# Performance work log

Measured on AMD Instinct MI355X. Metric: run time of the kernel, lower is better.

The kernel has to match this reference:

```python
import jax, jax.numpy as jnp
import numpy as np

S, B, H = 2048, 2, 2048
NP = 16            # num attention heads
HN = H // NP       # head dim = 128


def setup_inputs() -> dict:
    key = jax.random.key(0)
    k0, k1, k2 = jax.random.split(key, 3)
    hidden_states = jax.random.normal(k0, (S, B, H), dtype=jnp.float32) * 0.02
    w_qkv = jax.random.normal(k1, (3 * H, H), dtype=jnp.float32) * 0.02
    b_qkv = jnp.zeros((3 * H,), dtype=jnp.float32)
    w_dense = jax.random.normal(k2, (H, H), dtype=jnp.float32) * 0.02
    b_dense = jnp.zeros((H,), dtype=jnp.float32)
    # causal mask: True means "mask out" (strictly upper triangular)
    attention_mask = jnp.triu(jnp.ones((S, S), dtype=bool), k=1)[None, None]  # [1,1,S,S]
    return {
        "hidden_states": hidden_states,
        "attention_mask": attention_mask,
        "w_qkv": w_qkv,
        "b_qkv": b_qkv,
        "w_dense": w_dense,
        "b_dense": b_dense,
    }


def reference(hidden_states, attention_mask, w_qkv, b_qkv, w_dense, b_dense):
    s, b, h = hidden_states.shape
    # fused QKV projection (ColumnParallelLinear: y = x @ W^T + b)
    mixed = hidden_states @ w_qkv.T + b_qkv                 # [s,b,3h]
    mixed = mixed.reshape(s, b, NP, 3 * HN)
    q, k, v = jnp.split(mixed, 3, axis=-1)                  # each [s,b,np,hn]
    norm = 1.0 / jnp.sqrt(jnp.asarray(HN, hidden_states.dtype))
    # scaled QK^T -> [b,np,sq,sk]
    scores = jnp.einsum("sbnh,tbnh->bnst", q, k) * norm
    # attention_mask_func: masked_fill(mask, -10000.0)
    scores = jnp.where(attention_mask, jnp.asarray(-10000.0, scores.dtype), scores)
    # softmax in fp32 (softmax_in_fp32)
    probs = jax.nn.softmax(scores.astype(jnp.float32), axis=-1).astype(scores.dtype)
    # AV matmul -> [s,b,np,hn] -> [s,b,h]
    context = jnp.einsum("bnst,tbnh->sbnh", probs, v).reshape(s, b, h)
    # output projection (RowParallelLinear)
    out = context @ w_dense.T + b_dense
    return out
```

## Files before the change

kernel.cpp:

```cpp
#include <hip/hip_runtime.h>
#include <hip/hip_bf16.h>
#include <cstdint>
#include <cstddef>

#define SS   2048
#define BB   2
#define HH   2048
#define NHEAD 16
#define HDIM 128
#define H3   6144
#define MROWS 4096

typedef __attribute__((ext_vector_type(4))) float f32x4;
typedef __attribute__((ext_vector_type(8))) __bf16 bf16x8;
typedef __attribute__((ext_vector_type(8))) unsigned short us8;
typedef __attribute__((ext_vector_type(4))) unsigned short us4;

__device__ __forceinline__ unsigned short f2b(float f) {
    union { float f; unsigned u; } v; v.f = f;
    unsigned r = v.u + 0x7fffu + ((v.u >> 16) & 1u);
    return (unsigned short)(r >> 16);
}

__device__ __forceinline__ unsigned short f2b_hw(float f) {
    return __builtin_bit_cast(unsigned short, (__bf16)f);
}

__device__ __forceinline__ float exp2_fast(float x) {
    float r;
    asm("v_exp_f32 %0, %1" : "=v"(r) : "v"(x));
    return r;
}

__device__ __forceinline__ bf16x8 ld_b16x8(const unsigned short* p) {
    us8 u = *(const us8*)p;
    return __builtin_bit_cast(bf16x8, u);
}

__device__ __forceinline__ bf16x8 ld8_off(const unsigned short* base, int byteoff) {
    return __builtin_bit_cast(bf16x8, *(const us8*)((const char*)base + byteoff));
}

__device__ __forceinline__ int sw256(int b) { return b ^ (((b >> 8) & 7) << 4); }
__device__ __forceinline__ int sw128(int b) { return b ^ (((b >> 7) & 7) << 4); }

__device__ __forceinline__ void gload_lds16(const unsigned short* g, unsigned short* l) {
    __builtin_amdgcn_global_load_lds(
        (const __attribute__((address_space(1))) unsigned int*)g,
        (__attribute__((address_space(3))) unsigned int*)l, 16, 0, 0);
}

__global__ __launch_bounds__(256) void cvt_f32_bf16(
    const float* __restrict__ in, unsigned short* __restrict__ out, int n4)
{
    const int stride = gridDim.x * blockDim.x;
    for (int i = blockIdx.x * blockDim.x + threadIdx.x; i < n4; i += stride) {
        const float4 v = ((const float4*)in)[i];
        us4 o = { f2b(v.x), f2b(v.y), f2b(v.z), f2b(v.w) };
        ((us4*)out)[i] = o;
    }
}

__global__ __launch_bounds__(256) void transpose_v(
    const unsigned short* __restrict__ mixed,
    unsigned short* __restrict__ vt)
{
    const int st = blockIdx.x;
    const int nh = blockIdx.y;
    const int bb = blockIdx.z;
    const int tid = threadIdx.x;
    __shared__ unsigned short T[64][136];
#pragma unroll
    for (int i = 0; i < 4; ++i) {
        const int c = i * 256 + tid;
        const int sl = c >> 4, d0 = (c & 15) << 3;
        const us8 v = *(const us8*)(mixed +
            ((size_t)(st * 64 + sl) * BB + bb) * H3 + nh * 384 + 256 + d0);
        *(us8*)(&T[sl][d0]) = v;
    }
    __syncthreads();
#pragma unroll
    for (int i = 0; i < 4; ++i) {
        const int c = i * 256 + tid;
        const int d = c >> 3, sl0 = (c & 7) << 3;
        us8 o;
#pragma unroll
        for (int j = 0; j < 8; ++j) o[j] = T[sl0 + j][d];
        *(us8*)(vt + ((size_t)(bb * NHEAD + nh) * HDIM + d) * SS + st * 64 + sl0) = o;
    }
}

#define STAGE_UNIT(gp, lo)                                        \
    gload_lds16((gp) + soff[0], smem + (lo) + tid * 8);           \
    gload_lds16((gp) + soff[1], smem + (lo) + 4096 + tid * 8);

template <int BN, bool F32OUT>
__global__ __launch_bounds__(512, 2) void gemm_8ph(
    const unsigned short* __restrict__ A,
    const unsigned short* __restrict__ Bw,
    const float* __restrict__ bias,
    void* __restrict__ Cout,
    int Nv, int Kv)
{
    extern __shared__ unsigned short smem[];
    constexpr int NF     = BN / 64;
    constexpr int BUNITS = BN / 128;
    constexpr int BELEMS = BN * 64;

    const int tid  = threadIdx.x;
    const int lane = tid & 63;
    const int wave = tid >> 6;
    const int wm = wave >> 2, wn = wave & 3;
    const int bm = blockIdx.y, bn = blockIdx.x;

    const unsigned short* Ab = A  + (size_t)bm * 128 * Kv;
    const unsigned short* Bb = Bw + (size_t)bn * BN * Kv;

    int soff[2];
#pragma unroll
    for (int i = 0; i < 2; ++i) {
        const int p = (i * 512 + tid) * 16;
        const int l = p ^ (((p >> 7) & 7) << 4);
        soff[i] = (l >> 7) * Kv + ((l & 127) >> 1);
    }

    f32x4 acc[4][NF];
#pragma unroll
    for (int m = 0; m < 4; ++m)
#pragma unroll
        for (int n = 0; n < NF; ++n) acc[m][n] = (f32x4){0.f, 0.f, 0.f, 0.f};

    const int frow = lane & 15;
    const int g16  = (lane >> 4) << 4;
    const int swx  = (frow & 7) << 4;
    const int kx0  = g16 ^ swx;
    const int kx1  = (64 + g16) ^ swx;
    const int aRow = (wm * 64 + frow) * 128;
    const int bRow = 32768 + (wn * (BN / 4) + frow) * 128;

    const int NT = Kv >> 6;

    STAGE_UNIT(Ab, 0);
    STAGE_UNIT(Bb, 16384);
    STAGE_UNIT(Bb + 128 * Kv, 16384 + 8192);
    if constexpr (BUNITS == 3) { STAGE_UNIT(Bb + 256 * Kv, 16384 + 16384); }
    STAGE_UNIT(Bb + 64, 16384 + BELEMS);
    STAGE_UNIT(Bb + 128 * Kv + 64, 16384 + BELEMS + 8192);
    if constexpr (BUNITS == 3) { STAGE_UNIT(Bb + 256 * Kv + 64, 16384 + BELEMS + 16384); }
    if constexpr (BUNITS == 3) { asm volatile("s_waitcnt vmcnt(6)" ::: "memory"); }
    else                       { asm volatile("s_waitcnt vmcnt(4)" ::: "memory"); }
    __builtin_amdgcn_s_barrier();

    for (int t = 0; t < NT; ++t) {
        const int j  = t & 1;
        const int jn = j ^ 1;
        const int aj = j * 16384;
        const int bj = j * (BN * 128);
        const int cA = ((t + 1 < NT) ? (t + 1) : (NT - 1)) * 64;
        const int cB = ((t + 2 < NT) ? (t + 2) : (NT - 1)) * 64;

        bf16x8 bbf[NF][2];

        {
            bf16x8 a0 = ld8_off(smem, aj + aRow + 0 * 2048 + kx0);
            bf16x8 a1 = ld8_off(smem, aj + aRow + 0 * 2048 + kx1);
#pragma unroll
            for (int n = 0; n < NF; ++n) {
                bbf[n][0] = ld8_off(smem, bj + bRow + n * 2048 + kx0);
                bbf[n][1] = ld8_off(smem, bj + bRow + n * 2048 + kx1);
            }
            STAGE_UNIT(Ab + cA, jn * 8192);
            __builtin_amdgcn_s_barrier();
            asm volatile("s_waitcnt lgkmcnt(0)" ::: "memory");
            __builtin_amdgcn_sched_barrier(0);
            __builtin_amdgcn_s_setprio(1);
#pragma unroll
            for (int n = 0; n < NF; ++n) {
                acc[0][n] = __builtin_amdgcn_mfma_f32_16x16x32_bf16(a0, bbf[n][0], acc[0][n], 0, 0, 0);
                acc[0][n] = __builtin_amdgcn_mfma_f32_16x16x32_bf16(a1, bbf[n][1], acc[0][n], 0, 0, 0);
            }
            __builtin_amdgcn_s_setprio(0);
        }
        {
            bf16x8 a0 = ld8_off(smem, aj + aRow + 1 * 2048 + kx0);
            bf16x8 a1 = ld8_off(smem, aj + aRow + 1 * 2048 + kx1);
            STAGE_UNIT(Bb + cB, 16384 + j * BELEMS);
            __builtin_amdgcn_s_barrier();
            asm volatile("s_waitcnt lgkmcnt(0)" ::: "memory");
            __builtin_amdgcn_sched_barrier(0);
            __builtin_amdgcn_s_setprio(1);
#pragma unroll
            for (int n = 0; n < NF; ++n) {
                acc[1][n] = __builtin_amdgcn_mfma_f32_16x16x32_bf16(a0, bbf[n][0], acc[1][n], 0, 0, 0);
                acc[1][n] = __builtin_amdgcn_mfma_f32_16x16x32_bf16(a1, bbf[n][1], acc[1][n], 0, 0, 0);
            }
            __builtin_amdgcn_s_setprio(0);
        }
        {
            bf16x8 a0 = ld8_off(smem, aj + aRow + 2 * 2048 + kx0);
            bf16x8 a1 = ld8_off(smem, aj + aRow + 2 * 2048 + kx1);
            STAGE_UNIT(Bb + 128 * Kv + cB, 16384 + j * BELEMS + 8192);
            __builtin_amdgcn_s_barrier();
            asm volatile("s_waitcnt lgkmcnt(0)" ::: "memory");
            __builtin_amdgcn_sched_barrier(0);
            __builtin_amdgcn_s_setprio(1);
#pragma unroll
            for (int n = 0; n < NF; ++n) {
                acc[2][n] = __builtin_amdgcn_mfma_f32_16x16x32_bf16(a0, bbf[n][0], acc[2][n], 0, 0, 0);
                acc[2][n] = __builtin_amdgcn_mfma_f32_16x16x32_bf16(a1, bbf[n][1], acc[2][n], 0, 0, 0);
            }
            __builtin_amdgcn_s_setprio(0);
        }
        {
            bf16x8 a0 = ld8_off(smem, aj + aRow + 3 * 2048 + kx0);
            bf16x8 a1 = ld8_off(smem, aj + aRow + 3 * 2048 + kx1);
            if constexpr (BUNITS == 3) {
                STAGE_UNIT(Bb + 256 * Kv + cB, 16384 + j * BELEMS + 16384);
            }
            __builtin_amdgcn_s_barrier();
            asm volatile("s_waitcnt lgkmcnt(0)" ::: "memory");
            __builtin_amdgcn_sched_barrier(0);
            __builtin_amdgcn_s_setprio(1);
#pragma unroll
            for (int n = 0; n < NF; ++n) {
                acc[3][n] = __builtin_amdgcn_mfma_f32_16x16x32_bf16(a0, bbf[n][0], acc[3][n], 0, 0, 0);
                acc[3][n] = __builtin_amdgcn_mfma_f32_16x16x32_bf16(a1, bbf[n][1], acc[3][n], 0, 0, 0);
            }
            __builtin_amdgcn_s_setprio(0);
            if constexpr (BUNITS == 3) { asm volatile("s_waitcnt vmcnt(6)" ::: "memory"); }
            else                       { asm volatile("s_waitcnt vmcnt(4)" ::: "memory"); }
        }
    }

    const int r0 = (lane >> 4) << 2;
#pragma unroll
    for (int m = 0; m < 4; ++m) {
        const int row = bm * 128 + wm * 64 + m * 16 + r0;
#pragma unroll
        for (int n = 0; n < NF; ++n) {
            const int col = bn * BN + wn * (BN / 4) + n * 16 + frow;
            const float bv = bias[col];
            float scale = 1.0f;
            if constexpr (!F32OUT) {
                if ((col % 384) < 128)
                    scale = (float)(0.08838834764831843 * 1.4426950408889634);
            }
#pragma unroll
            for (int r = 0; r < 4; ++r) {
                const float o = (acc[m][n][r] + bv) * scale;
                if (F32OUT) ((float*)Cout)[(size_t)(row + r) * Nv + col] = o;
                else        ((unsigned short*)Cout)[(size_t)(row + r) * Nv + col] = f2b(o);
            }
        }
    }
}

__global__ __launch_bounds__(256) void attn_kernel(
    const unsigned short* __restrict__ mixed,
    const unsigned short* __restrict__ vt,
    unsigned short* __restrict__ context)
{
    const int id   = blockIdx.x;
    const int c    = id & 7;
    const int k    = id >> 3;
    const int pair = k & 15;
    const int nhbb = c + 8 * (k >> 4);
    const int nh   = nhbb >> 1;
    const int bb   = nhbb & 1;

    const int tid  = threadIdx.x;
    const int lane = tid & 63;
    const int wave = tid >> 6;

    __shared__ __align__(1024) unsigned short smem[16384 + 16384 + 4096];

    const int frow = lane & 15;
    const int g16  = (lane >> 4) << 4;
    const int r0   = (lane >> 4) << 2;

    int koff[4], voff[4];
#pragma unroll
    for (int i = 0; i < 4; ++i) {
        const int p0 = (i * 256 + tid) * 16;
        const int lK = p0 ^ (((p0 >> 8) & 7) << 4);
        koff[i] = (lK >> 8) * (BB * H3) + ((lK & 255) >> 1);
        const int lV = p0 ^ (((p0 >> 7) & 7) << 4);
        voff[i] = (lV >> 7) * SS + ((lV & 127) >> 1);
    }

    const unsigned short* kg = mixed + (size_t)bb * H3 + nh * 384 + 128;
    const unsigned short* vg = vt + (size_t)(bb * NHEAD + nh) * HDIM * SS;

    char* Pb = (char*)(smem + 32768) + wave * 2048;

    for (int half = 0; half < 2; ++half) {
        const int qt = half ? (31 - pair) : pair;
        const int q0 = qt * 64 + wave * 16;

        bf16x8 qf[4];
        {
            const unsigned short* qptr =
                mixed + ((size_t)(q0 + frow) * BB + bb) * H3 + nh * 384;
#pragma unroll
            for (int kk = 0; kk < 4; ++kk)
                qf[kk] = ld_b16x8(qptr + kk * 32 + ((lane >> 4) << 3));
        }

        f32x4 Oacc[8];
#pragma unroll
        for (int ct = 0; ct < 8; ++ct) Oacc[ct] = (f32x4){0.f, 0.f, 0.f, 0.f};
        float m_r[4] = {-1e30f, -1e30f, -1e30f, -1e30f};
        float l_r[4] = {0.f, 0.f, 0.f, 0.f};

        {
            unsigned short* Kd = smem + wave * 512;
            unsigned short* Vd = smem + 16384 + wave * 512;
#pragma unroll
            for (int i = 0; i < 4; ++i) {
                gload_lds16(kg + koff[i], Kd + i * 2048);
                gload_lds16(vg + voff[i], Vd + i * 2048);
            }
        }
        __syncthreads();

        int cur = 0;
        for (int kt = 0; kt <= qt; ++kt) {
            if (kt < qt) {
                const unsigned short* kt_g = kg + (size_t)(kt + 1) * 64 * (BB * H3);
                const unsigned short* vt_g = vg + (kt + 1) * 64;
                unsigned short* Kd = smem + (cur ^ 1) * 8192 + wave * 512;
                unsigned short* Vd = smem + 16384 + (cur ^ 1) * 8192 + wave * 512;
#pragma unroll
                for (int i = 0; i < 4; ++i) {
                    gload_lds16(kt_g + koff[i], Kd + i * 2048);
                    gload_lds16(vt_g + voff[i], Vd + i * 2048);
                }
            }

            const unsigned short* Ks = smem + cur * 8192;
            const unsigned short* Vs = smem + 16384 + cur * 8192;

            f32x4 sc4[4];
#pragma unroll
            for (int t = 0; t < 4; ++t) {
                f32x4 s = (f32x4){0.f, 0.f, 0.f, 0.f};
#pragma unroll
                for (int kk = 0; kk < 4; ++kk) {
                    bf16x8 kf = ld8_off(Ks, sw256((t * 16 + frow) * 256 + kk * 64 + g16));
                    s = __builtin_amdgcn_mfma_f32_16x16x32_bf16(qf[kk], kf, s, 0, 0, 0);
                }
                sc4[t] = s;
            }

            if (kt == qt) {
#pragma unroll
                for (int t = 0; t < 4; ++t) {
                    const int kcol = qt * 64 + t * 16 + frow;
#pragma unroll
                    for (int r = 0; r < 4; ++r)
                        if (kcol > q0 + r0 + r) sc4[t][r] = -1e30f;
                }
            }

            float pmax[4];
#pragma unroll
            for (int r = 0; r < 4; ++r)
                pmax[r] = fmaxf(fmaxf(sc4[0][r], sc4[1][r]), fmaxf(sc4[2][r], sc4[3][r]));
            bool need = false;
#pragma unroll
            for (int r = 0; r < 4; ++r) need = need || (pmax[r] > m_r[r] + 11.5f);
            if (__any(need)) {
                float tmax[4];
#pragma unroll
                for (int r = 0; r < 4; ++r) {
                    tmax[r] = pmax[r];
                    tmax[r] = fmaxf(tmax[r], __shfl_xor(tmax[r], 1, 64));
                    tmax[r] = fmaxf(tmax[r], __shfl_xor(tmax[r], 2, 64));
                    tmax[r] = fmaxf(tmax[r], __shfl_xor(tmax[r], 4, 64));
                    tmax[r] = fmaxf(tmax[r], __shfl_xor(tmax[r], 8, 64));
                }
                float a_r[4];
#pragma unroll
                for (int r = 0; r < 4; ++r) {
                    const float mnew = fmaxf(m_r[r], tmax[r]);
                    a_r[r] = exp2_fast(m_r[r] - mnew);
                    m_r[r] = mnew;
                    l_r[r] *= a_r[r];
                }
#pragma unroll
                for (int ct = 0; ct < 8; ++ct)
#pragma unroll
                    for (int r = 0; r < 4; ++r) Oacc[ct][r] *= a_r[r];
            }

            float rsum[4] = {0.f, 0.f, 0.f, 0.f};
#pragma unroll
            for (int t = 0; t < 4; ++t)
#pragma unroll
                for (int r = 0; r < 4; ++r) {
                    const float p = exp2_fast(sc4[t][r] - m_r[r]);
                    sc4[t][r] = p;
                    rsum[r] += p;
                }
#pragma unroll
            for (int r = 0; r < 4; ++r) {
                rsum[r] += __shfl_xor(rsum[r], 1, 64);
                rsum[r] += __shfl_xor(rsum[r], 2, 64);
                rsum[r] += __shfl_xor(rsum[r], 4, 64);
                rsum[r] += __shfl_xor(rsum[r], 8, 64);
                l_r[r] += rsum[r];
            }

#pragma unroll
            for (int t = 0; t < 4; ++t)
#pragma unroll
                for (int r = 0; r < 4; ++r)
                    *(unsigned short*)(Pb + sw128((r0 + r) * 128 + (t * 16 + frow) * 2)) =
                        f2b_hw(sc4[t][r]);

#pragma unroll
            for (int ks = 0; ks < 2; ++ks) {
                bf16x8 pf = ld8_off((const unsigned short*)Pb, sw128(frow * 128 + ks * 64 + g16));
#pragma unroll
                for (int ct = 0; ct < 8; ++ct) {
                    bf16x8 vf = ld8_off(Vs, sw128((ct * 16 + frow) * 128 + ks * 64 + g16));
                    Oacc[ct] = __builtin_amdgcn_mfma_f32_16x16x32_bf16(pf, vf, Oacc[ct], 0, 0, 0);
                }
            }

            __syncthreads();
            cur ^= 1;
        }

#pragma unroll
        for (int ct = 0; ct < 8; ++ct) {
            const int d = ct * 16 + frow;
#pragma unroll
            for (int r = 0; r < 4; ++r) {
                const float o = Oacc[ct][r] / l_r[r];
                const size_t row = (size_t)(q0 + r0 + r) * BB + bb;
                context[row * HH + nh * 128 + d] = f2b_hw(o);
            }
        }
    }
}

extern "C" void kernel_launch(void* const* d_in, const int* in_sizes, int n_in,
                              void* d_out, int out_size, void* d_ws, size_t ws_size,
                              hipStream_t stream) {
    const float* hidden  = (const float*)d_in[0];
    const float* w_qkv   = (const float*)d_in[2];
    const float* b_qkv   = (const float*)d_in[3];
    const float* w_dense = (const float*)d_in[4];
    const float* b_dense = (const float*)d_in[5];
    float* out = (float*)d_out;

    unsigned short* mixed = (unsigned short*)d_ws;
    unsigned short* hb    = mixed + (size_t)MROWS * H3;
    unsigned short* wq    = hb + (size_t)MROWS * HH;
    unsigned short* wd    = wq + (size_t)H3 * HH;
    unsigned short* context = hb;
    unsigned short* vtg     = wq;

    dim3 blk(256);
    cvt_f32_bf16<<<2048, blk, 0, stream>>>(hidden, hb, (MROWS * HH) / 4);
    cvt_f32_bf16<<<2048, blk, 0, stream>>>(w_qkv, wq, (H3 * HH) / 4);
    cvt_f32_bf16<<<1024, blk, 0, stream>>>(w_dense, wd, (HH * HH) / 4);

    hipFuncSetAttribute(reinterpret_cast<const void*>(gemm_8ph<384, false>),
                        hipFuncAttributeMaxDynamicSharedMemorySize, 131072);
    gemm_8ph<384, false><<<dim3(H3 / 384, MROWS / 128), dim3(512), 131072, stream>>>(
        hb, wq, b_qkv, mixed, H3, HH);
    transpose_v<<<dim3(32, NHEAD, BB), blk, 0, stream>>>(mixed, vtg);
    attn_kernel<<<dim3(512), blk, 0, stream>>>(mixed, vtg, context);
    hipFuncSetAttribute(reinterpret_cast<const void*>(gemm_8ph<256, true>),
                        hipFuncAttributeMaxDynamicSharedMemorySize, 98304);
    gemm_8ph<256, true><<<dim3(HH / 256, MROWS / 128), dim3(512), 98304, stream>>>(
        context, wd, b_dense, out, HH, HH);
}
```

Measured before the change: 251.3 us.

## Process both paired query tiles in one KV sweep to share K/V loads

The attention kernel used to handle its two causal-balanced query tiles one after the other, loading K/V tiles twice. Now it keeps two sets of Q fragments, accumulators and softmax state, and runs a single KV loop to the larger tile. Each loaded K/V tile feeds both query tiles, which halves the global-to-LDS traffic and the barriers for the shared prefix. The cost is roughly double the accumulator registers, which may lower occupancy or cause spills. The final normalisation also switches from a division to a hardware reciprocal.

```diff
diff --git a/kernel.cpp b/kernel.cpp
--- a/kernel.cpp
+++ b/kernel.cpp
@@ -255,6 +255,100 @@
     }
 }
 
+__device__ __forceinline__ void attn_tile(
+    const unsigned short* Ks, const unsigned short* Vs, char* Pb,
+    const bf16x8 (&qf)[4], f32x4 (&Oacc)[8], float (&m_r)[4], float (&l_r)[4],
+    bool diag, int wrow, int frow, int g16, int r0)
+{
+    f32x4 sc4[4];
+#pragma unroll
+    for (int t = 0; t < 4; ++t) {
+        f32x4 s = (f32x4){0.f, 0.f, 0.f, 0.f};
+#pragma unroll
+        for (int kk = 0; kk < 4; ++kk) {
+            bf16x8 kf = ld8_off(Ks, sw256((t * 16 + frow) * 256 + kk * 64 + g16));
+            s = __builtin_amdgcn_mfma_f32_16x16x32_bf16(qf[kk], kf, s, 0, 0, 0);
+        }
+        sc4[t] = s;
+    }
+
+    if (diag) {
+#pragma unroll
+        for (int t = 0; t < 4; ++t) {
+            const int kc = t * 16 + frow;
+#pragma unroll
+            for (int r = 0; r < 4; ++r)
+                if (kc > wrow + r) sc4[t][r] = -1e30f;
+        }
+    }
+
+    float pmax[4];
+#pragma unroll
+    for (int r = 0; r < 4; ++r)
+        pmax[r] = fmaxf(fmaxf(sc4[0][r], sc4[1][r]), fmaxf(sc4[2][r], sc4[3][r]));
+    bool need = false;
+#pragma unroll
+    for (int r = 0; r < 4; ++r) need = need || (pmax[r] > m_r[r] + 11.5f);
+    if (__any(need)) {
+        float tmax[4];
+#pragma unroll
+        for (int r = 0; r < 4; ++r) {
+            tmax[r] = pmax[r];
+            tmax[r] = fmaxf(tmax[r], __shfl_xor(tmax[r], 1, 64));
+            tmax[r] = fmaxf(tmax[r], __shfl_xor(tmax[r], 2, 64));
+            tmax[r] = fmaxf(tmax[r], __shfl_xor(tmax[r], 4, 64));
+            tmax[r] = fmaxf(tmax[r], __shfl_xor(tmax[r], 8, 64));
+        }
+        float a_r[4];
+#pragma unroll
+        for (int r = 0; r < 4; ++r) {
+            const float mnew = fmaxf(m_r[r], tmax[r]);
+            a_r[r] = exp2_fast(m_r[r] - mnew);
+            m_r[r] = mnew;
+            l_r[r] *= a_r[r];
+        }
+#pragma unroll
+        for (int ct = 0; ct < 8; ++ct)
+#pragma unroll
+            for (int r = 0; r < 4; ++r) Oacc[ct][r] *= a_r[r];
+    }
+
+    float rsum[4] = {0.f, 0.f, 0.f, 0.f};
+#pragma unroll
+    for (int t = 0; t < 4; ++t)
+#pragma unroll
+        for (int r = 0; r < 4; ++r) {
+            const float p = exp2_fast(sc4[t][r] - m_r[r]);
+            sc4[t][r] = p;
+            rsum[r] += p;
+        }
+#pragma unroll
+    for (int r = 0; r < 4; ++r) {
+        rsum[r] += __shfl_xor(rsum[r], 1, 64);
+        rsum[r] += __shfl_xor(rsum[r], 2, 64);
+        rsum[r] += __shfl_xor(rsum[r], 4, 64);
+        rsum[r] += __shfl_xor(rsum[r], 8, 64);
+        l_r[r] += rsum[r];
+    }
+
+#pragma unroll
+    for (int t = 0; t < 4; ++t)
+#pragma unroll
+        for (int r = 0; r < 4; ++r)
+            *(unsigned short*)(Pb + sw128((r0 + r) * 128 + (t * 16 + frow) * 2)) =
+                f2b_hw(sc4[t][r]);
+
+#pragma unroll
+    for (int ks = 0; ks < 2; ++ks) {
+        bf16x8 pf = ld8_off((const unsigned short*)Pb, sw128(frow * 128 + ks * 64 + g16));
+#pragma unroll
+        for (int ct = 0; ct < 8; ++ct) {
+            bf16x8 vf = ld8_off(Vs, sw128((ct * 16 + frow) * 128 + ks * 64 + g16));
+            Oacc[ct] = __builtin_amdgcn_mfma_f32_16x16x32_bf16(pf, vf, Oacc[ct], 0, 0, 0);
+        }
+    }
+}
+
 __global__ __launch_bounds__(256) void attn_kernel(
     const unsigned short* __restrict__ mixed,
     const unsigned short* __restrict__ vt,
@@ -268,6 +362,9 @@
     const int nh   = nhbb >> 1;
     const int bb   = nhbb & 1;
 
+    const int qtA = pair;
+    const int qtB = 31 - pair;
+
     const int tid  = threadIdx.x;
     const int lane = tid & 63;
     const int wave = tid >> 6;
@@ -277,6 +374,7 @@
     const int frow = lane & 15;
     const int g16  = (lane >> 4) << 4;
     const int r0   = (lane >> 4) << 2;
+    const int wrow = wave * 16 + r0;
 
     int koff[4], voff[4];
 #pragma unroll
@@ -293,153 +391,86 @@
 
     char* Pb = (char*)(smem + 32768) + wave * 2048;
 
-    for (int half = 0; half < 2; ++half) {
-        const int qt = half ? (31 - pair) : pair;
-        const int q0 = qt * 64 + wave * 16;
-
-        bf16x8 qf[4];
-        {
-            const unsigned short* qptr =
-                mixed + ((size_t)(q0 + frow) * BB + bb) * H3 + nh * 384;
-#pragma unroll
-            for (int kk = 0; kk < 4; ++kk)
-                qf[kk] = ld_b16x8(qptr + kk * 32 + ((lane >> 4) << 3));
-        }
-
-        f32x4 Oacc[8];
-#pragma unroll
-        for (int ct = 0; ct < 8; ++ct) Oacc[ct] = (f32x4){0.f, 0.f, 0.f, 0.f};
-        float m_r[4] = {-1e30f, -1e30f, -1e30f, -1e30f};
-        float l_r[4] = {0.f, 0.f, 0.f, 0.f};
-
-        {
-            unsigned short* Kd = smem + wave * 512;
-            unsigned short* Vd = smem + 16384 + wave * 512;
+    bf16x8 qfA[4], qfB[4];
+    {
+        const int q0A = qtA * 64 + wave * 16;
+        const int q0B = qtB * 64 + wave * 16;
+        const unsigned short* qpA =
+            mixed + ((size_t)(q0A + frow) * BB + bb) * H3 + nh * 384;
+        const unsigned short* qpB =
+            mixed + ((size_t)(q0B + frow) * BB + bb) * H3 + nh * 384;
+#pragma unroll
+        for (int kk = 0; kk < 4; ++kk) {
+            qfA[kk] = ld_b16x8(qpA + kk * 32 + ((lane >> 4) << 3));
+            qfB[kk] = ld_b16x8(qpB + kk * 32 + ((lane >> 4) << 3));
+        }
+    }
+
+    f32x4 OA[8], OB[8];
+#pragma unroll
+    for (int ct = 0; ct < 8; ++ct) {
+        OA[ct] = (f32x4){0.f, 0.f, 0.f, 0.f};
+        OB[ct] = (f32x4){0.f, 0.f, 0.f, 0.f};
+    }
+    float mA[4] = {-1e30f, -1e30f, -1e30f, -1e30f};
+    float lA[4] = {0.f, 0.f, 0.f, 0.f};
+    float mB[4] = {-1e30f, -1e30f, -1e30f, -1e30f};
+    float lB[4] = {0.f, 0.f, 0.f, 0.f};
+
+    {
+        unsigned short* Kd = smem + wave * 512;
+        unsigned short* Vd = smem + 16384 + wave * 512;
+#pragma unroll
+        for (int i = 0; i < 4; ++i) {
+            gload_lds16(kg + koff[i], Kd + i * 2048);
+            gload_lds16(vg + voff[i], Vd + i * 2048);
+        }
+    }
+    __syncthreads();
+
+    int cur = 0;
+    for (int kt = 0; kt <= qtB; ++kt) {
+        if (kt < qtB) {
+            const unsigned short* kt_g = kg + (size_t)(kt + 1) * 64 * (BB * H3);
+            const unsigned short* vt_g = vg + (kt + 1) * 64;
+            unsigned short* Kd = smem + (cur ^ 1) * 8192 + wave * 512;
+            unsigned short* Vd = smem + 16384 + (cur ^ 1) * 8192 + wave * 512;
 #pragma unroll
             for (int i = 0; i < 4; ++i) {
-                gload_lds16(kg + koff[i], Kd + i * 2048);
-                gload_lds16(vg + voff[i], Vd + i * 2048);
-            }
-        }
+                gload_lds16(kt_g + koff[i], Kd + i * 2048);
+                gload_lds16(vt_g + voff[i], Vd + i * 2048);
+            }
+        }
+
+        const unsigned short* Ks = smem + cur * 8192;
+        const unsigned short* Vs = smem + 16384 + cur * 8192;
+
+        attn_tile(Ks, Vs, Pb, qfB, OB, mB, lB, kt == qtB, wrow, frow, g16, r0);
+        if (kt <= qtA)
+            attn_tile(Ks, Vs, Pb, qfA, OA, mA, lA, kt == qtA, wrow, frow, g16, r0);
+
         __syncthreads();
-
-        int cur = 0;
-        for (int kt = 0; kt <= qt; ++kt) {
-            if (kt < qt) {
-                const unsigned short* kt_g = kg + (size_t)(kt + 1) * 64 * (BB * H3);
-                const unsigned short* vt_g = vg + (kt + 1) * 64;
-                unsigned short* Kd = smem + (cur ^ 1) * 8192 + wave * 512;
-                unsigned short* Vd = smem + 16384 + (cur ^ 1) * 8192 + wave * 512;
-#pragma unroll
-                for (int i = 0; i < 4; ++i) {
-                    gload_lds16(kt_g + koff[i], Kd + i * 2048);
-                    gload_lds16(vt_g + voff[i], Vd + i * 2048);
-                }
-            }
-
-            const unsigned short* Ks = smem + cur * 8192;
-            const unsigned short* Vs = smem + 16384 + cur * 8192;
-
-            f32x4 sc4[4];
-#pragma unroll
-            for (int t = 0; t < 4; ++t) {
-                f32x4 s = (f32x4){0.f, 0.f, 0.f, 0.f};
-#pragma unroll
-                for (int kk = 0; kk < 4; ++kk) {
-                    bf16x8 kf = ld8_off(Ks, sw256((t * 16 + frow) * 256 + kk * 64 + g16));
-                    s = __builtin_amdgcn_mfma_f32_16x16x32_bf16(qf[kk], kf, s, 0, 0, 0);
-                }
-                sc4[t] = s;
-            }
-
-            if (kt == qt) {
-#pragma unroll
-                for (int t = 0; t < 4; ++t) {
-                    const int kcol = qt * 64 + t * 16 + frow;
-#pragma unroll
-                    for (int r = 0; r < 4; ++r)
-                        if (kcol > q0 + r0 + r) sc4[t][r] = -1e30f;
-                }
-            }
-
-            float pmax[4];
-#pragma unroll
-            for (int r = 0; r < 4; ++r)
-                pmax[r] = fmaxf(fmaxf(sc4[0][r], sc4[1][r]), fmaxf(sc4[2][r], sc4[3][r]));
-            bool need = false;
-#pragma unroll
-            for (int r = 0; r < 4; ++r) need = need || (pmax[r] > m_r[r] + 11.5f);
-            if (__any(need)) {
-                float tmax[4];
-#pragma unroll
-                for (int r = 0; r < 4; ++r) {
-                    tmax[r] = pmax[r];
-                    tmax[r] = fmaxf(tmax[r], __shfl_xor(tmax[r], 1, 64));
-                    tmax[r] = fmaxf(tmax[r], __shfl_xor(tmax[r], 2, 64));
-                    tmax[r] = fmaxf(tmax[r], __shfl_xor(tmax[r], 4, 64));
-                    tmax[r] = fmaxf(tmax[r], __shfl_xor(tmax[r], 8, 64));
-                }
-                float a_r[4];
-#pragma unroll
-                for (int r = 0; r < 4; ++r) {
-                    const float mnew = fmaxf(m_r[r], tmax[r]);
-                    a_r[r] = exp2_fast(m_r[r] - mnew);
-                    m_r[r] = mnew;
-                    l_r[r] *= a_r[r];
-                }
-#pragma unroll
-                for (int ct = 0; ct < 8; ++ct)
-#pragma unroll
-                    for (int r = 0; r < 4; ++r) Oacc[ct][r] *= a_r[r];
-            }
-
-            float rsum[4] = {0.f, 0.f, 0.f, 0.f};
-#pragma unroll
-            for (int t = 0; t < 4; ++t)
-#pragma unroll
-                for (int r = 0; r < 4; ++r) {
-                    const float p = exp2_fast(sc4[t][r] - m_r[r]);
-                    sc4[t][r] = p;
-                    rsum[r] += p;
-                }
-#pragma unroll
-            for (int r = 0; r < 4; ++r) {
-                rsum[r] += __shfl_xor(rsum[r], 1, 64);
-                rsum[r] += __shfl_xor(rsum[r], 2, 64);
-                rsum[r] += __shfl_xor(rsum[r], 4, 64);
-                rsum[r] += __shfl_xor(rsum[r], 8, 64);
-                l_r[r] += rsum[r];
-            }
-
-#pragma unroll
-            for (int t = 0; t < 4; ++t)
-#pragma unroll
-                for (int r = 0; r < 4; ++r)
-                    *(unsigned short*)(Pb + sw128((r0 + r) * 128 + (t * 16 + frow) * 2)) =
-                        f2b_hw(sc4[t][r]);
-
-#pragma unroll
-            for (int ks = 0; ks < 2; ++ks) {
-                bf16x8 pf = ld8_off((const unsigned short*)Pb, sw128(frow * 128 + ks * 64 + g16));
-#pragma unroll
-                for (int ct = 0; ct < 8; ++ct) {
-                    bf16x8 vf = ld8_off(Vs, sw128((ct * 16 + frow) * 128 + ks * 64 + g16));
-                    Oacc[ct] = __builtin_amdgcn_mfma_f32_16x16x32_bf16(pf, vf, Oacc[ct], 0, 0, 0);
-                }
-            }
-
-            __syncthreads();
-            cur ^= 1;
-        }
-
+        cur ^= 1;
+    }
+
+    {
+        const int q0A = qtA * 64 + wave * 16;
+        const int q0B = qtB * 64 + wave * 16;
+        float rlA[4], rlB[4];
+#pragma unroll
+        for (int r = 0; r < 4; ++r) {
+            rlA[r] = __builtin_amdgcn_rcpf(lA[r]);
+            rlB[r] = __builtin_amdgcn_rcpf(lB[r]);
+        }
 #pragma unroll
         for (int ct = 0; ct < 8; ++ct) {
             const int d = ct * 16 + frow;
 #pragma unroll
             for (int r = 0; r < 4; ++r) {
-                const float o = Oacc[ct][r] / l_r[r];
-                const size_t row = (size_t)(q0 + r0 + r) * BB + bb;
-                context[row * HH + nh * 128 + d] = f2b_hw(o);
+                const size_t rowA = (size_t)(q0A + r0 + r) * BB + bb;
+                const size_t rowB = (size_t)(q0B + r0 + r) * BB + bb;
+                context[rowA * HH + nh * 128 + d] = f2b_hw(OA[ct][r] * rlA[r]);
+                context[rowB * HH + nh * 128 + d] = f2b_hw(OB[ct][r] * rlB[r]);
             }
         }
     }
```

After: 280.5 us. 1.12x slower.
